# Kernel tuning notes

Hardware: AMD Instinct MI355X
Metric: run time of the kernel (lower is better)

Reference implementation:

```python
import jax, jax.numpy as jnp
import numpy as np

MAX_DEGREE = 8
IN_CH = 64
OUT_CH = 64
N_SH = 45  # number of even-degree SH coefficients up to degree 8
BATCH = 2048


def make_ls(max_degree, n_sh):
    ls = np.zeros(n_sh, dtype=np.int32)
    for degree in range(0, max_degree + 1, 2):
        for order in range(-degree, degree + 1):
            ls[int(0.5 * degree * (degree + 1) + order)] = degree
    return ls


def setup_inputs() -> dict:
    key = jax.random.key(0)
    k1, k2 = jax.random.split(key)
    x = jax.random.normal(k1, (BATCH, IN_CH, N_SH), dtype=jnp.float32)
    # xavier_uniform over (out, in, max_degree/2+1)
    fan_in, fan_out = IN_CH, OUT_CH
    bound = float(np.sqrt(6.0 / (fan_in + fan_out)))
    weights = jax.random.uniform(k2, (OUT_CH, IN_CH, MAX_DEGREE // 2 + 1),
                                 dtype=jnp.float32, minval=-bound, maxval=bound)
    ls = jnp.asarray(make_ls(MAX_DEGREE, N_SH))
    return {"x": x, "weights": weights, "ls": ls}


def reference(x, weights, ls):
    # per-coefficient scale sqrt(pi / (2l + 1)), shape (n_sh,)
    scale = jnp.sqrt(jnp.pi / (2.0 * ls.astype(x.dtype) + 1.0))
    # gather per-degree weights to per-coefficient weights: (out, in, n_sh)
    w = weights[:, :, ls // 2] * scale  # fold scale into weights (tiny tensor)
    # contract over input channels without materializing (B, out, in, n_sh)
    return jnp.einsum('oic,bic->boc', w, x)
```

## Files before the change

### kernel.cpp

```cpp
#include <hip/hip_runtime.h>

#define BATCH 2048
#define IC 64
#define OC 64
#define NSH 45
#define NSH_PAD 48
#define BT 16
#define CG 8
#define NCG 6
#define NBT (BATCH / BT)
#define XTOT ((size_t)BATCH * IC * NSH)
#define WF_ELEMS (NSH_PAD * IC * OC)
#define PI_F 3.14159265358979323846f

#define C_STRIDE 1060
#define BG_STRIDE 528

typedef float f4u __attribute__((ext_vector_type(4), aligned(4)));

__global__ __launch_bounds__(256) void fold_kernel(const float* __restrict__ w,
                                                   const int* __restrict__ ls,
                                                   float* __restrict__ wf) {
    int idx = blockIdx.x * 256 + threadIdx.x;
    int o = idx & 63;
    int i = (idx >> 6) & 63;
    int c = idx >> 12;
    float v = 0.0f;
    if (c < NSH) {
        int l = ls[c];
        float sc = sqrtf(PI_F / (2.0f * (float)l + 1.0f));
        v = w[(o * IC + i) * 5 + (l >> 1)] * sc;
    }
    wf[idx] = v;
}

template <bool FOLDED>
__global__ __launch_bounds__(128) void sph_kernel(const float* __restrict__ x,
                                                  const float* __restrict__ w,
                                                  const int* __restrict__ ls,
                                                  float* __restrict__ out) {
    __shared__ float xs[CG * C_STRIDE];

    const int bid = blockIdx.x;
    const int xcd  = bid & 7;
    const int slot = bid >> 3;
    const int q    = slot / NCG;
    const int cg   = slot - q * NCG;
    const int bt   = xcd * 16 + q;
    const int cb   = cg * CG;
    const int tid  = threadIdx.x;

    const size_t xbase0 = (size_t)bt * (BT * IC * NSH);
#pragma unroll
    for (int k = 0; k < 16; ++k) {
        int s  = k * 128 + tid;
        int ch = s & 1;
        int bb = (s >> 1) & 15;
        int ii = s >> 5;
        int c0 = ch * 4;
        size_t g = xbase0 + (size_t)bb * (IC * NSH) + (size_t)ii * NSH + cb + c0;
        f4u v;
        if (g + 3 < XTOT) {
            v = *(const f4u*)(x + g);
        } else {
            v.x = (g + 0 < XTOT) ? x[g + 0] : 0.0f;
            v.y = (g + 1 < XTOT) ? x[g + 1] : 0.0f;
            v.z = (g + 2 < XTOT) ? x[g + 2] : 0.0f;
            v.w = (g + 3 < XTOT) ? x[g + 3] : 0.0f;
        }
        int bg   = bb >> 3;
        int bl   = bb & 7;
        int base = bg * BG_STRIDE + ii * 8 + bl;
        xs[(c0 + 0) * C_STRIDE + base] = v.x;
        xs[(c0 + 1) * C_STRIDE + base] = v.y;
        xs[(c0 + 2) * C_STRIDE + base] = v.z;
        xs[(c0 + 3) * C_STRIDE + base] = v.w;
    }
    __syncthreads();

    const int bg = tid & 1;
    const int og = (tid >> 1) & 7;
    const int ci = tid >> 4;
    const int c  = cb + ci;
    const int o0 = og * 8;

    float acc[8][8];
#pragma unroll
    for (int a = 0; a < 8; ++a)
#pragma unroll
        for (int b = 0; b < 8; ++b) acc[a][b] = 0.0f;

    const float* xp = xs + ci * C_STRIDE + bg * BG_STRIDE;

    if (FOLDED) {
        const float* wp = w + ((size_t)c * IC) * OC + o0;
#pragma unroll 4
        for (int i = 0; i < IC; ++i) {
            float4 xa = *(const float4*)(xp + i * 8);
            float4 xb = *(const float4*)(xp + i * 8 + 4);
            float4 wa = *(const float4*)(wp + i * OC);
            float4 wb = *(const float4*)(wp + i * OC + 4);
            float xv[8] = {xa.x, xa.y, xa.z, xa.w, xb.x, xb.y, xb.z, xb.w};
            float wv[8] = {wa.x, wa.y, wa.z, wa.w, wb.x, wb.y, wb.z, wb.w};
#pragma unroll
            for (int a = 0; a < 8; ++a)
#pragma unroll
                for (int b = 0; b < 8; ++b)
                    acc[a][b] = fmaf(xv[a], wv[b], acc[a][b]);
        }
    } else {
        int l2c = ls[c < NSH ? c : NSH - 1] >> 1;
        const float* wp = w + (size_t)o0 * (IC * 5) + l2c;
#pragma unroll 2
        for (int i = 0; i < IC; ++i) {
            float4 xa = *(const float4*)(xp + i * 8);
            float4 xb = *(const float4*)(xp + i * 8 + 4);
            float xv[8] = {xa.x, xa.y, xa.z, xa.w, xb.x, xb.y, xb.z, xb.w};
            float wv[8];
#pragma unroll
            for (int u = 0; u < 8; ++u) wv[u] = wp[(size_t)u * (IC * 5) + i * 5];
#pragma unroll
            for (int a = 0; a < 8; ++a)
#pragma unroll
                for (int b = 0; b < 8; ++b)
                    acc[a][b] = fmaf(xv[a], wv[b], acc[a][b]);
        }
    }

    if (c < NSH) {
        float sc = 1.0f;
        if (!FOLDED) {
            int l = ls[c];
            sc = sqrtf(PI_F / (2.0f * (float)l + 1.0f));
        }
        size_t orow = ((size_t)(bt * BT + bg * 8) * OC + o0) * NSH + c;
#pragma unroll
        for (int a = 0; a < 8; ++a) {
#pragma unroll
            for (int b = 0; b < 8; ++b) {
                float r = FOLDED ? acc[a][b] : acc[a][b] * sc;
                out[orow + (size_t)a * (OC * NSH) + (size_t)b * NSH] = r;
            }
        }
    }
}

extern "C" void kernel_launch(void* const* d_in, const int* in_sizes, int n_in,
                              void* d_out, int out_size, void* d_ws, size_t ws_size,
                              hipStream_t stream) {
    const float* x  = (const float*)d_in[0];
    const float* wt = (const float*)d_in[1];
    const int*   ls = (const int*)d_in[2];
    float* out = (float*)d_out;

    const int nblocks = NBT * NCG;

    if (ws_size >= (size_t)WF_ELEMS * sizeof(float)) {
        float* wf = (float*)d_ws;
        fold_kernel<<<WF_ELEMS / 256, 256, 0, stream>>>(wt, ls, wf);
        sph_kernel<true><<<nblocks, 128, 0, stream>>>(x, wf, ls, out);
    } else {
        sph_kernel<false><<<nblocks, 128, 0, stream>>>(x, wt, ls, out);
    }
}
```

Before: 100.8 us.

## Drop LDS staging and retile to read x directly with vectorized output stores

Removes the shared-memory staging of x and the syncthreads barrier. Each thread now reads x straight from global memory and accumulates a 4-batch by 2-output by 4-coefficient tile. The grid is retiled into 32-batch by 16-output by 8-coefficient blocks, which lets output be written as 4-wide vectors along the contiguous coefficient axis instead of strided scalar stores. The fold kernel now writes 4-wide vectors and no longer pads to 48 coefficients. The trade-off is more redundant global and L2 reads of x across the four output tiles, lower FMA-per-load reuse, and overlapping coefficient ranges in the last tile (41..44), which compute some results twice.

```diff
diff --git a/kernel.cpp b/kernel.cpp
--- a/kernel.cpp
+++ b/kernel.cpp
@@ -1,147 +1,139 @@
 #include <hip/hip_runtime.h>
 
-#define BATCH 2048
 #define IC 64
 #define OC 64
 #define NSH 45
-#define NSH_PAD 48
-#define BT 16
-#define CG 8
-#define NCG 6
-#define NBT (BATCH / BT)
-#define XTOT ((size_t)BATCH * IC * NSH)
-#define WF_ELEMS (NSH_PAD * IC * OC)
+#define BATCH 2048
 #define PI_F 3.14159265358979323846f
+#define WF_FLOATS (NSH * IC * OC)
 
-#define C_STRIDE 1060
-#define BG_STRIDE 528
-
-typedef float f4u __attribute__((ext_vector_type(4), aligned(4)));
+typedef float f4a4 __attribute__((ext_vector_type(4), aligned(4)));
+typedef float f2a8 __attribute__((ext_vector_type(2), aligned(8)));
 
 __global__ __launch_bounds__(256) void fold_kernel(const float* __restrict__ w,
                                                    const int* __restrict__ ls,
                                                    float* __restrict__ wf) {
-    int idx = blockIdx.x * 256 + threadIdx.x;
-    int o = idx & 63;
-    int i = (idx >> 6) & 63;
-    int c = idx >> 12;
-    float v = 0.0f;
-    if (c < NSH) {
-        int l = ls[c];
-        float sc = sqrtf(PI_F / (2.0f * (float)l + 1.0f));
-        v = w[(o * IC + i) * 5 + (l >> 1)] * sc;
-    }
-    wf[idx] = v;
+    int t = blockIdx.x * 256 + threadIdx.x;
+    if (t >= NSH * IC * 16) return;
+    int o4 = t & 15;
+    int i  = (t >> 4) & 63;
+    int c  = t >> 10;
+    int l  = ls[c];
+    int l2 = l >> 1;
+    float sc = sqrtf(PI_F / (2.0f * (float)l + 1.0f));
+    int o0 = o4 * 4;
+    f4a4 v;
+    v[0] = w[((o0 + 0) * IC + i) * 5 + l2] * sc;
+    v[1] = w[((o0 + 1) * IC + i) * 5 + l2] * sc;
+    v[2] = w[((o0 + 2) * IC + i) * 5 + l2] * sc;
+    v[3] = w[((o0 + 3) * IC + i) * 5 + l2] * sc;
+    *(f4a4*)(wf + ((size_t)c * IC + i) * OC + o0) = v;
 }
 
 template <bool FOLDED>
-__global__ __launch_bounds__(128) void sph_kernel(const float* __restrict__ x,
-                                                  const float* __restrict__ w,
-                                                  const int* __restrict__ ls,
-                                                  float* __restrict__ out) {
-    __shared__ float xs[CG * C_STRIDE];
+__global__ __launch_bounds__(128) void sph_main(const float* __restrict__ x,
+                                                const float* __restrict__ w,
+                                                const int* __restrict__ ls,
+                                                float* __restrict__ out) {
+    int wg  = (int)(blockIdx.x & 7) * 192 + (int)(blockIdx.x >> 3);
+    int bt  = wg / 24;
+    int rem = wg - bt * 24;
+    int ot  = rem / 6;
+    int ct  = rem - ot * 6;
 
-    const int bid = blockIdx.x;
-    const int xcd  = bid & 7;
-    const int slot = bid >> 3;
-    const int q    = slot / NCG;
-    const int cg   = slot - q * NCG;
-    const int bt   = xcd * 16 + q;
-    const int cb   = cg * CG;
-    const int tid  = threadIdx.x;
+    int tid = threadIdx.x;
+    int cq  = tid & 1;
+    int og  = (tid >> 1) & 7;
+    int bq  = tid >> 4;
 
-    const size_t xbase0 = (size_t)bt * (BT * IC * NSH);
+    int cqg = ct * 2 + cq;
+    int c0  = cqg < 11 ? cqg * 4 : 41;
+    int o0  = ot * 16 + og * 2;
+    int b0  = bt * 32 + bq * 4;
+
+    float acc[4][2][4];
 #pragma unroll
-    for (int k = 0; k < 16; ++k) {
-        int s  = k * 128 + tid;
-        int ch = s & 1;
-        int bb = (s >> 1) & 15;
-        int ii = s >> 5;
-        int c0 = ch * 4;
-        size_t g = xbase0 + (size_t)bb * (IC * NSH) + (size_t)ii * NSH + cb + c0;
-        f4u v;
-        if (g + 3 < XTOT) {
-            v = *(const f4u*)(x + g);
-        } else {
-            v.x = (g + 0 < XTOT) ? x[g + 0] : 0.0f;
-            v.y = (g + 1 < XTOT) ? x[g + 1] : 0.0f;
-            v.z = (g + 2 < XTOT) ? x[g + 2] : 0.0f;
-            v.w = (g + 3 < XTOT) ? x[g + 3] : 0.0f;
-        }
-        int bg   = bb >> 3;
-        int bl   = bb & 7;
-        int base = bg * BG_STRIDE + ii * 8 + bl;
-        xs[(c0 + 0) * C_STRIDE + base] = v.x;
-        xs[(c0 + 1) * C_STRIDE + base] = v.y;
-        xs[(c0 + 2) * C_STRIDE + base] = v.z;
-        xs[(c0 + 3) * C_STRIDE + base] = v.w;
-    }
-    __syncthreads();
+    for (int bb = 0; bb < 4; ++bb)
+#pragma unroll
+        for (int oo = 0; oo < 2; ++oo)
+#pragma unroll
+            for (int cc = 0; cc < 4; ++cc) acc[bb][oo][cc] = 0.0f;
 
-    const int bg = tid & 1;
-    const int og = (tid >> 1) & 7;
-    const int ci = tid >> 4;
-    const int c  = cb + ci;
-    const int o0 = og * 8;
-
-    float acc[8][8];
-#pragma unroll
-    for (int a = 0; a < 8; ++a)
-#pragma unroll
-        for (int b = 0; b < 8; ++b) acc[a][b] = 0.0f;
-
-    const float* xp = xs + ci * C_STRIDE + bg * BG_STRIDE;
+    const float* xp = x + (size_t)b0 * (IC * NSH) + c0;
 
     if (FOLDED) {
-        const float* wp = w + ((size_t)c * IC) * OC + o0;
+        const float* wp = w + (size_t)c0 * (IC * OC) + o0;
 #pragma unroll 4
         for (int i = 0; i < IC; ++i) {
-            float4 xa = *(const float4*)(xp + i * 8);
-            float4 xb = *(const float4*)(xp + i * 8 + 4);
-            float4 wa = *(const float4*)(wp + i * OC);
-            float4 wb = *(const float4*)(wp + i * OC + 4);
-            float xv[8] = {xa.x, xa.y, xa.z, xa.w, xb.x, xb.y, xb.z, xb.w};
-            float wv[8] = {wa.x, wa.y, wa.z, wa.w, wb.x, wb.y, wb.z, wb.w};
+            float xv[4][4];
+            float wv[4][2];
 #pragma unroll
-            for (int a = 0; a < 8; ++a)
+            for (int bb = 0; bb < 4; ++bb) {
+                f4a4 v = *(const f4a4*)(xp + bb * (IC * NSH) + i * NSH);
+                xv[bb][0] = v[0]; xv[bb][1] = v[1]; xv[bb][2] = v[2]; xv[bb][3] = v[3];
+            }
 #pragma unroll
-                for (int b = 0; b < 8; ++b)
-                    acc[a][b] = fmaf(xv[a], wv[b], acc[a][b]);
+            for (int cc = 0; cc < 4; ++cc) {
+                f2a8 v = *(const f2a8*)(wp + cc * (IC * OC) + i * OC);
+                wv[cc][0] = v[0]; wv[cc][1] = v[1];
+            }
+#pragma unroll
+            for (int bb = 0; bb < 4; ++bb)
+#pragma unroll
+                for (int oo = 0; oo < 2; ++oo)
+#pragma unroll
+                    for (int cc = 0; cc < 4; ++cc)
+                        acc[bb][oo][cc] = fmaf(xv[bb][cc], wv[cc][oo], acc[bb][oo][cc]);
         }
+#pragma unroll
+        for (int bb = 0; bb < 4; ++bb)
+#pragma unroll
+            for (int oo = 0; oo < 2; ++oo) {
+                f4a4 r;
+                r[0] = acc[bb][oo][0]; r[1] = acc[bb][oo][1];
+                r[2] = acc[bb][oo][2]; r[3] = acc[bb][oo][3];
+                *(f4a4*)(out + ((size_t)(b0 + bb) * OC + (o0 + oo)) * NSH + c0) = r;
+            }
     } else {
-        int l2c = ls[c < NSH ? c : NSH - 1] >> 1;
-        const float* wp = w + (size_t)o0 * (IC * 5) + l2c;
+        int l2c[4]; float scl[4];
+#pragma unroll
+        for (int cc = 0; cc < 4; ++cc) {
+            int l = ls[c0 + cc];
+            l2c[cc] = l >> 1;
+            scl[cc] = sqrtf(PI_F / (2.0f * (float)l + 1.0f));
+        }
 #pragma unroll 2
         for (int i = 0; i < IC; ++i) {
-            float4 xa = *(const float4*)(xp + i * 8);
-            float4 xb = *(const float4*)(xp + i * 8 + 4);
-            float xv[8] = {xa.x, xa.y, xa.z, xa.w, xb.x, xb.y, xb.z, xb.w};
-            float wv[8];
+            float xv[4][4];
+            float wv[4][2];
 #pragma unroll
-            for (int u = 0; u < 8; ++u) wv[u] = wp[(size_t)u * (IC * 5) + i * 5];
+            for (int bb = 0; bb < 4; ++bb) {
+                f4a4 v = *(const f4a4*)(xp + bb * (IC * NSH) + i * NSH);
+                xv[bb][0] = v[0]; xv[bb][1] = v[1]; xv[bb][2] = v[2]; xv[bb][3] = v[3];
+            }
 #pragma unroll
-            for (int a = 0; a < 8; ++a)
+            for (int cc = 0; cc < 4; ++cc) {
 #pragma unroll
-                for (int b = 0; b < 8; ++b)
-                    acc[a][b] = fmaf(xv[a], wv[b], acc[a][b]);
+                for (int oo = 0; oo < 2; ++oo)
+                    wv[cc][oo] = w[((size_t)(o0 + oo) * IC + i) * 5 + l2c[cc]];
+            }
+#pragma unroll
+            for (int bb = 0; bb < 4; ++bb)
+#pragma unroll
+                for (int oo = 0; oo < 2; ++oo)
+#pragma unroll
+                    for (int cc = 0; cc < 4; ++cc)
+                        acc[bb][oo][cc] = fmaf(xv[bb][cc], wv[cc][oo], acc[bb][oo][cc]);
         }
-    }
-
-    if (c < NSH) {
-        float sc = 1.0f;
-        if (!FOLDED) {
-            int l = ls[c];
-            sc = sqrtf(PI_F / (2.0f * (float)l + 1.0f));
-        }
-        size_t orow = ((size_t)(bt * BT + bg * 8) * OC + o0) * NSH + c;
 #pragma unroll
-        for (int a = 0; a < 8; ++a) {
+        for (int bb = 0; bb < 4; ++bb)
 #pragma unroll
-            for (int b = 0; b < 8; ++b) {
-                float r = FOLDED ? acc[a][b] : acc[a][b] * sc;
-                out[orow + (size_t)a * (OC * NSH) + (size_t)b * NSH] = r;
+            for (int oo = 0; oo < 2; ++oo) {
+                f4a4 r;
+                r[0] = acc[bb][oo][0] * scl[0]; r[1] = acc[bb][oo][1] * scl[1];
+                r[2] = acc[bb][oo][2] * scl[2]; r[3] = acc[bb][oo][3] * scl[3];
+                *(f4a4*)(out + ((size_t)(b0 + bb) * OC + (o0 + oo)) * NSH + c0) = r;
             }
-        }
     }
 }
 
@@ -153,13 +145,13 @@
     const int*   ls = (const int*)d_in[2];
     float* out = (float*)d_out;
 
-    const int nblocks = NBT * NCG;
+    const int nblocks = 64 * 4 * 6;
 
-    if (ws_size >= (size_t)WF_ELEMS * sizeof(float)) {
+    if (ws_size >= (size_t)WF_FLOATS * sizeof(float)) {
         float* wf = (float*)d_ws;
-        fold_kernel<<<WF_ELEMS / 256, 256, 0, stream>>>(wt, ls, wf);
-        sph_kernel<true><<<nblocks, 128, 0, stream>>>(x, wf, ls, out);
+        fold_kernel<<<(NSH * IC * 16) / 256, 256, 0, stream>>>(wt, ls, wf);
+        sph_main<true><<<nblocks, 128, 0, stream>>>(x, wf, ls, out);
     } else {
-        sph_kernel<false><<<nblocks, 128, 0, stream>>>(x, wt, ls, out);
+        sph_main<false><<<nblocks, 128, 0, stream>>>(x, wt, ls, out);
     }
 }
```

Result: slower. 145.8 us (+44.7%).
